# Optimization experiments

Measured on AMD Instinct MI355X. Metric: run time of the kernel, lower is better.

## Reference

```python
import jax, jax.numpy as jnp
import numpy as np

N = 8192          # number of nodes
DIN = 512         # in_features
DOUT = 256        # out_features
P_EDGE = 0.004    # ~32 avg degree
NEG_INF = -9e15   # matches the torch module's -9000000000000000.0 mask value


def setup_inputs() -> dict:
    key = jax.random.key(0)
    ks = jax.random.split(key, 7)
    x = jax.random.normal(ks[0], (N, DIN), dtype=jnp.float32)
    # binary adjacency, Bernoulli(P_EDGE)
    adj = (jax.random.uniform(ks[1], (N, N)) < P_EDGE).astype(jnp.float32)
    W1 = jax.random.normal(ks[2], (DIN, DOUT), dtype=jnp.float32) * 0.05
    b1 = jnp.zeros((DOUT,), dtype=jnp.float32)
    a1_w = jax.random.normal(ks[3], (DOUT,), dtype=jnp.float32) * 0.05
    a1_b = jnp.zeros((), dtype=jnp.float32)
    a2_w = jax.random.normal(ks[4], (DOUT,), dtype=jnp.float32) * 0.05
    a2_b = jnp.zeros((), dtype=jnp.float32)
    return {"x": x, "adj": adj, "W1": W1, "b1": b1,
            "a1_w": a1_w, "a1_b": a1_b, "a2_w": a2_w, "a2_b": a2_b}


def reference(x, adj, W1, b1, a1_w, a1_b, a2_w, a2_b):
    # h = linear1(elu(x))                       [n, DOUT]
    h = jnp.matmul(jax.nn.elu(x), W1) + b1
    # per-node scalar scores g1 (source/col) and g2 (dest/row)
    g1 = h @ a1_w + a1_b                       # [n]
    g2 = h @ a2_w + a2_b                       # [n]
    # kron trick collapses to: scores[i,j] = adj[i,j] * (g2[i] + g1[j])
    scores = adj * (g2[:, None] + g1[None, :])  # [n, n]
    e = jax.nn.leaky_relu(scores, negative_slope=0.2)
    attention = jax.nn.softmax(jnp.where(adj > 0, e, NEG_INF), axis=1)
    # untied=False path: weighted aggregation of h (dropout p=0 is identity)
    return attention @ h
```

## Files before the change

kernel.cpp:

```cpp
#include <hip/hip_runtime.h>
#include <hip/hip_bf16.h>
#include <cstdint>
#include <cstddef>

#define N_NODES 8192
#define DIN 512
#define DOUT 256
#define CAP 128
#define GEMM_BLKS 512
#define SCAN_BLKS 2048

typedef short bf16x8 __attribute__((ext_vector_type(8)));
typedef float f32x4 __attribute__((ext_vector_type(4)));
typedef unsigned int u32x4 __attribute__((ext_vector_type(4)));

__device__ __forceinline__ float bf2f(unsigned short u) {
    union { unsigned int ui; float f; } v; v.ui = ((unsigned int)u) << 16; return v.f;
}
__device__ __forceinline__ unsigned short f2bf(float f) {
    union { float f; unsigned int u; } v; v.f = f;
    unsigned int u = v.u;
    return (unsigned short)((u + 0x7fffu + ((u >> 16) & 1u)) >> 16);
}
__device__ __forceinline__ float elu1(float v) { return v > 0.f ? v : (expf(v) - 1.f); }

__global__ __launch_bounds__(256) void convw_kernel(
    const float* __restrict__ W1, unsigned short* __restrict__ wb, int* __restrict__ ecnt)
{
    const int n = blockIdx.x;
    const int k = threadIdx.x * 2;
    unsigned short a = f2bf(W1[(size_t)k * DOUT + n]);
    unsigned short b = f2bf(W1[(size_t)(k + 1) * DOUT + n]);
    *(unsigned int*)(wb + (size_t)n * DIN + k) = (unsigned int)a | ((unsigned int)b << 16);
    if (blockIdx.x < 32) ecnt[blockIdx.x * 256 + threadIdx.x] = 0;
}

__global__ __launch_bounds__(256) void fused_kernel(
    const float* __restrict__ x, const unsigned short* __restrict__ wb,
    const float* __restrict__ b1,
    const float* __restrict__ a1w, const float* __restrict__ a1b,
    const float* __restrict__ a2w, const float* __restrict__ a2b,
    unsigned short* __restrict__ h, float* __restrict__ g1, float* __restrict__ g2,
    const float* __restrict__ adj, int* __restrict__ ecnt, int* __restrict__ ecols)
{
    const int tid = threadIdx.x;

    if (blockIdx.x < GEMM_BLKS) {
        const int wave = tid >> 6, lane = tid & 63;
        const int quad = lane >> 4, r16 = lane & 15;
        const int m0 = blockIdx.x * 16;
        const int n0 = wave * 64;

        f32x4 acc[4] = {{0.f,0.f,0.f,0.f},{0.f,0.f,0.f,0.f},{0.f,0.f,0.f,0.f},{0.f,0.f,0.f,0.f}};
        const float* xrow = x + (size_t)(m0 + r16) * DIN;

        for (int k0 = 0; k0 < DIN; k0 += 32) {
            const int kb = k0 + quad * 8;
            float4 f0 = *(const float4*)(xrow + kb);
            float4 f1 = *(const float4*)(xrow + kb + 4);
            bf16x8 A;
            A[0] = (short)f2bf(elu1(f0.x)); A[1] = (short)f2bf(elu1(f0.y));
            A[2] = (short)f2bf(elu1(f0.z)); A[3] = (short)f2bf(elu1(f0.w));
            A[4] = (short)f2bf(elu1(f1.x)); A[5] = (short)f2bf(elu1(f1.y));
            A[6] = (short)f2bf(elu1(f1.z)); A[7] = (short)f2bf(elu1(f1.w));
            bf16x8 B[4];
            #pragma unroll
            for (int s = 0; s < 4; ++s)
                B[s] = *(const bf16x8*)(wb + (size_t)(n0 + s * 16 + r16) * DIN + kb);
            #pragma unroll
            for (int ni = 0; ni < 4; ++ni)
                acc[ni] = __builtin_amdgcn_mfma_f32_16x16x32_bf16(A, B[ni], acc[ni], 0, 0, 0);
        }

        float p1[4] = {0.f, 0.f, 0.f, 0.f};
        float p2[4] = {0.f, 0.f, 0.f, 0.f};
        #pragma unroll
        for (int ni = 0; ni < 4; ++ni) {
            const int col = n0 + ni * 16 + r16;
            const float bias = b1[col];
            const float w1c = a1w[col], w2c = a2w[col];
            #pragma unroll
            for (int rr = 0; rr < 4; ++rr) {
                float val = acc[ni][rr] + bias;
                h[(size_t)(m0 + quad * 4 + rr) * DOUT + col] = f2bf(val);
                p1[rr] += val * w1c;
                p2[rr] += val * w2c;
            }
        }
        #pragma unroll
        for (int off = 1; off < 16; off <<= 1) {
            #pragma unroll
            for (int rr = 0; rr < 4; ++rr) {
                p1[rr] += __shfl_xor(p1[rr], off, 64);
                p2[rr] += __shfl_xor(p2[rr], off, 64);
            }
        }
        __shared__ float sg1[16][4];
        __shared__ float sg2[16][4];
        if (r16 == 0) {
            #pragma unroll
            for (int rr = 0; rr < 4; ++rr) {
                sg1[quad * 4 + rr][wave] = p1[rr];
                sg2[quad * 4 + rr][wave] = p2[rr];
            }
        }
        __syncthreads();
        if (tid < 16) {
            float t1 = sg1[tid][0] + sg1[tid][1] + sg1[tid][2] + sg1[tid][3];
            float t2 = sg2[tid][0] + sg2[tid][1] + sg2[tid][2] + sg2[tid][3];
            g1[m0 + tid] = t1 + a1b[0];
            g2[m0 + tid] = t2 + a2b[0];
        }
        return;
    }

    const int b = blockIdx.x - GEMM_BLKS;
    const u32x4* a4 = (const u32x4*)adj;
    const int base = b * 256 + tid;
    const int stride = SCAN_BLKS * 256;

    #pragma unroll 1
    for (int g = 0; g < 4; ++g) {
        u32x4 raws[8];
        #pragma unroll
        for (int c = 0; c < 8; ++c)
            raws[c] = __builtin_nontemporal_load(a4 + (size_t)base + (size_t)(g * 8 + c) * stride);
        #pragma unroll
        for (int c = 0; c < 8; ++c) {
            u32x4 raw = raws[c];
            if (raw.x | raw.y | raw.z | raw.w) {
                unsigned int wv[4] = {raw.x, raw.y, raw.z, raw.w};
                const int fbase = (base + (g * 8 + c) * stride) * 4;
                #pragma unroll
                for (int q = 0; q < 4; ++q) {
                    if (wv[q]) {
                        int idx = fbase + q;
                        int i   = idx >> 13;
                        int col = idx & 8191;
                        int pos = atomicAdd(&ecnt[i], 1);
                        if (pos < CAP) ecols[(size_t)i * CAP + pos] = col;
                    }
                }
            }
        }
    }
}

__global__ __launch_bounds__(256) void agg2_kernel(
    const int* __restrict__ ecnt, const int* __restrict__ ecols,
    const unsigned short* __restrict__ h,
    const float* __restrict__ g1, const float* __restrict__ g2,
    float* __restrict__ out)
{
    __shared__ float evs[4][CAP];
    __shared__ int   jls[4][CAP];

    const int tid  = threadIdx.x;
    const int w    = tid >> 6;
    const int lane = tid & 63;
    const int i    = blockIdx.x * 4 + w;

    int K = ecnt[i];
    if (K > CAP) K = CAP;
    const float g2i = g2[i];

    if (K == 0) {
        f32x4 acc = {0.f, 0.f, 0.f, 0.f};
        for (int j = 0; j < N_NODES; ++j) {
            ushort4 hv = *(const ushort4*)(h + (size_t)j * DOUT + lane * 4);
            acc[0] += bf2f(hv.x); acc[1] += bf2f(hv.y);
            acc[2] += bf2f(hv.z); acc[3] += bf2f(hv.w);
        }
        const float sc = 1.f / (float)N_NODES;
        float4 o = {acc[0] * sc, acc[1] * sc, acc[2] * sc, acc[3] * sc};
        *(float4*)(out + (size_t)i * DOUT + lane * 4) = o;
        return;
    }

    float e0 = -1e30f, e1 = -1e30f;
    int   j0 = 0,      j1 = 0;
    if (lane < K) {
        j0 = ecols[(size_t)i * CAP + lane];
        float s = g2i + g1[j0];
        e0 = s > 0.f ? s : 0.2f * s;
    }
    if (lane + 64 < K) {
        j1 = ecols[(size_t)i * CAP + lane + 64];
        float s = g2i + g1[j1];
        e1 = s > 0.f ? s : 0.2f * s;
    }
    float m = fmaxf(e0, e1);
    #pragma unroll
    for (int off = 32; off > 0; off >>= 1) m = fmaxf(m, __shfl_xor(m, off, 64));

    float p0 = expf(e0 - m);
    float p1 = expf(e1 - m);
    float ssum = p0 + p1;
    #pragma unroll
    for (int off = 32; off > 0; off >>= 1) ssum += __shfl_xor(ssum, off, 64);
    const float inv = 1.f / ssum;

    evs[w][lane] = p0;      jls[w][lane] = j0;
    evs[w][lane + 64] = p1; jls[w][lane + 64] = j1;

    const unsigned short* hp = h + lane * 4;
    f32x4 accA = {0.f, 0.f, 0.f, 0.f};
    f32x4 accB = {0.f, 0.f, 0.f, 0.f};
    int k = 0;
    for (; k + 4 <= K; k += 4) {
        float q0 = evs[w][k],   q1 = evs[w][k+1], q2 = evs[w][k+2], q3 = evs[w][k+3];
        int   i0 = jls[w][k],   i1 = jls[w][k+1], i2 = jls[w][k+2], i3 = jls[w][k+3];
        ushort4 h0 = *(const ushort4*)(hp + (size_t)i0 * DOUT);
        ushort4 h1 = *(const ushort4*)(hp + (size_t)i1 * DOUT);
        ushort4 h2 = *(const ushort4*)(hp + (size_t)i2 * DOUT);
        ushort4 h3 = *(const ushort4*)(hp + (size_t)i3 * DOUT);
        accA[0] += q0 * bf2f(h0.x); accA[1] += q0 * bf2f(h0.y);
        accA[2] += q0 * bf2f(h0.z); accA[3] += q0 * bf2f(h0.w);
        accB[0] += q1 * bf2f(h1.x); accB[1] += q1 * bf2f(h1.y);
        accB[2] += q1 * bf2f(h1.z); accB[3] += q1 * bf2f(h1.w);
        accA[0] += q2 * bf2f(h2.x); accA[1] += q2 * bf2f(h2.y);
        accA[2] += q2 * bf2f(h2.z); accA[3] += q2 * bf2f(h2.w);
        accB[0] += q3 * bf2f(h3.x); accB[1] += q3 * bf2f(h3.y);
        accB[2] += q3 * bf2f(h3.z); accB[3] += q3 * bf2f(h3.w);
    }
    for (; k < K; ++k) {
        float q = evs[w][k];
        ushort4 hv = *(const ushort4*)(hp + (size_t)jls[w][k] * DOUT);
        accA[0] += q * bf2f(hv.x); accA[1] += q * bf2f(hv.y);
        accA[2] += q * bf2f(hv.z); accA[3] += q * bf2f(hv.w);
    }
    float4 o = {(accA[0] + accB[0]) * inv, (accA[1] + accB[1]) * inv,
                (accA[2] + accB[2]) * inv, (accA[3] + accB[3]) * inv};
    *(float4*)(out + (size_t)i * DOUT + lane * 4) = o;
}

extern "C" void kernel_launch(void* const* d_in, const int* in_sizes, int n_in,
                              void* d_out, int out_size, void* d_ws, size_t ws_size,
                              hipStream_t stream) {
    const float* x   = (const float*)d_in[0];
    const float* adj = (const float*)d_in[1];
    const float* W1  = (const float*)d_in[2];
    const float* b1  = (const float*)d_in[3];
    const float* a1w = (const float*)d_in[4];
    const float* a1b = (const float*)d_in[5];
    const float* a2w = (const float*)d_in[6];
    const float* a2b = (const float*)d_in[7];

    char* w = (char*)d_ws;
    float* g1 = (float*)w;                     w += (size_t)N_NODES * 4;
    float* g2 = (float*)w;                     w += (size_t)N_NODES * 4;
    unsigned short* h  = (unsigned short*)w;   w += (size_t)N_NODES * DOUT * 2;
    unsigned short* wb = (unsigned short*)w;   w += (size_t)DOUT * DIN * 2;
    int* ecnt = (int*)w;                       w += (size_t)N_NODES * 4;
    int* ecols = (int*)w;
    float* out = (float*)d_out;

    hipLaunchKernelGGL(convw_kernel, dim3(256), dim3(256), 0, stream, W1, wb, ecnt);
    hipLaunchKernelGGL(fused_kernel, dim3(GEMM_BLKS + SCAN_BLKS), dim3(256), 0, stream,
                       x, wb, b1, a1w, a1b, a2w, a2b, h, g1, g2, adj, ecnt, ecols);
    hipLaunchKernelGGL(agg2_kernel, dim3(2048), dim3(256), 0, stream, ecnt, ecols, h, g1, g2, out);
}
```

Measured before the change: 420.0 us.

## Build per-row edge lists with wave-local LDS atomics instead of global atomics

Result: faster. 390.6 us, median of 2 (-7.0%).

```diff
diff --git a/kernel.cpp b/kernel.cpp
--- a/kernel.cpp
+++ b/kernel.cpp
@@ -25,14 +25,13 @@
 __device__ __forceinline__ float elu1(float v) { return v > 0.f ? v : (expf(v) - 1.f); }
 
 __global__ __launch_bounds__(256) void convw_kernel(
-    const float* __restrict__ W1, unsigned short* __restrict__ wb, int* __restrict__ ecnt)
+    const float* __restrict__ W1, unsigned short* __restrict__ wb)
 {
     const int n = blockIdx.x;
     const int k = threadIdx.x * 2;
     unsigned short a = f2bf(W1[(size_t)k * DOUT + n]);
     unsigned short b = f2bf(W1[(size_t)(k + 1) * DOUT + n]);
     *(unsigned int*)(wb + (size_t)n * DIN + k) = (unsigned int)a | ((unsigned int)b << 16);
-    if (blockIdx.x < 32) ecnt[blockIdx.x * 256 + threadIdx.x] = 0;
 }
 
 __global__ __launch_bounds__(256) void fused_kernel(
@@ -114,36 +113,46 @@
         return;
     }
 
-    const int b = blockIdx.x - GEMM_BLKS;
-    const u32x4* a4 = (const u32x4*)adj;
-    const int base = b * 256 + tid;
-    const int stride = SCAN_BLKS * 256;
+    __shared__ int eidx[4][CAP];
+    __shared__ int wcnt[4];
+
+    const int w    = tid >> 6;
+    const int lane = tid & 63;
+    const int i    = (blockIdx.x - GEMM_BLKS) * 4 + w;
+
+    if (lane == 0) wcnt[w] = 0;
+
+    const float* arow = adj + (size_t)i * N_NODES;
 
     #pragma unroll 1
     for (int g = 0; g < 4; ++g) {
         u32x4 raws[8];
         #pragma unroll
         for (int c = 0; c < 8; ++c)
-            raws[c] = __builtin_nontemporal_load(a4 + (size_t)base + (size_t)(g * 8 + c) * stride);
+            raws[c] = __builtin_nontemporal_load(
+                (const u32x4*)(arow + (g * 8 + c) * 256 + lane * 4));
         #pragma unroll
         for (int c = 0; c < 8; ++c) {
             u32x4 raw = raws[c];
             if (raw.x | raw.y | raw.z | raw.w) {
                 unsigned int wv[4] = {raw.x, raw.y, raw.z, raw.w};
-                const int fbase = (base + (g * 8 + c) * stride) * 4;
                 #pragma unroll
                 for (int q = 0; q < 4; ++q) {
                     if (wv[q]) {
-                        int idx = fbase + q;
-                        int i   = idx >> 13;
-                        int col = idx & 8191;
-                        int pos = atomicAdd(&ecnt[i], 1);
-                        if (pos < CAP) ecols[(size_t)i * CAP + pos] = col;
+                        int j = (g * 8 + c) * 256 + lane * 4 + q;
+                        int pos = atomicAdd(&wcnt[w], 1);
+                        if (pos < CAP) eidx[w][pos] = j;
                     }
                 }
             }
         }
     }
+
+    int K = wcnt[w];
+    if (K > CAP) K = CAP;
+    if (lane == 0) ecnt[i] = K;
+    for (int k = lane; k < K; k += 64)
+        ecols[(size_t)i * CAP + k] = eidx[w][k];
 }
 
 __global__ __launch_bounds__(256) void agg2_kernel(
@@ -255,7 +264,7 @@
     int* ecols = (int*)w;
     float* out = (float*)d_out;
 
-    hipLaunchKernelGGL(convw_kernel, dim3(256), dim3(256), 0, stream, W1, wb, ecnt);
+    hipLaunchKernelGGL(convw_kernel, dim3(256), dim3(256), 0, stream, W1, wb);
     hipLaunchKernelGGL(fused_kernel, dim3(GEMM_BLKS + SCAN_BLKS), dim3(256), 0, stream,
                        x, wb, b1, a1w, a1b, a2w, a2b, h, g1, g2, adj, ecnt, ecols);
     hipLaunchKernelGGL(agg2_kernel, dim3(2048), dim3(256), 0, stream, ecnt, ecols, h, g1, g2, out);
```
